# Performance work log

Hardware: AMD Instinct MI355X
Metric: run time of the kernel (lower is better)

Reference implementation:

```python
import jax, jax.numpy as jnp
import numpy as np

B, M, C = 8, 8192, 256   # batch, seeds, seed feature dim
F = 128                  # vote feature dim
P, K = 256, 32           # proposals, samples per group
CA, NCLS = 256, 10       # aggregated feat dim, classes
RADIUS = 0.3


def _lin(x, w, b):
    # 1x1 conv == pointwise linear; w: (out, in)
    return jnp.einsum('...c,oc->...o', x, w) + b


def _bnrelu(x, s, t):
    # eval-mode BatchNorm folded to per-channel affine, then ReLU
    return jnp.maximum(x * s + t, 0.0)


def _fps(xyz, npoint):
    # farthest point sampling; deterministic start at index 0
    Bb, N, _ = xyz.shape
    bidx = jnp.arange(Bb)

    def step(carry, _):
        distance, farthest = carry
        centroid = xyz[bidx, farthest][:, None, :]          # (B,1,2)
        d = jnp.sum((xyz - centroid) ** 2, -1)              # (B,N)
        distance = jnp.minimum(distance, d)
        return (distance, jnp.argmax(distance, -1)), farthest

    init = (jnp.full((Bb, N), 1e10, xyz.dtype), jnp.zeros((Bb,), jnp.int32))
    _, idx = jax.lax.scan(step, init, None, length=npoint)
    return jnp.transpose(idx)                               # (B, npoint)


def _ball_query(xyz, new_xyz, radius, nsample):
    # squared-distance cdist (monotone in euclid dist, so same sort order)
    N = xyz.shape[1]
    d2 = (jnp.sum(new_xyz ** 2, -1)[:, :, None]
          + jnp.sum(xyz ** 2, -1)[:, None, :]
          - 2.0 * jnp.einsum('bsd,bnd->bsn', new_xyz, xyz))  # (B,S,N)
    gidx = jnp.broadcast_to(jnp.arange(N), d2.shape)
    # out-of-radius points replaced by group_first (= index 0, as in source)
    gidx = jnp.where(d2 > radius * radius, 0, gidx)
    order = jnp.argsort(d2, axis=-1)
    return jnp.take_along_axis(gidx, order, axis=-1)[:, :, :nsample]


def _gather(points, idx):
    # points: (B,N,C); idx: (B,...) -> (B,...,C)
    return jax.vmap(lambda p, i: p[i])(points, idx)


def _forward(seed_xyz, seed_feats,
             v_off_w1, v_off_b1, v_off_s1, v_off_t1, v_off_w2, v_off_b2,
             v_ft_w1, v_ft_b1, v_ft_s1, v_ft_t1, v_ft_w2, v_ft_b2,
             a_w1, a_b1, a_s1, a_t1, a_w2, a_b2, a_s2, a_t2,
             p_w1, p_b1, p_s1, p_t1, p_w2, p_b2, p_s2, p_t2,
             obj_w, obj_b, cls_w, cls_b):
    # --- VotingModule (vote_factor=1) ---
    h = _bnrelu(_lin(seed_feats, v_off_w1, v_off_b1), v_off_s1, v_off_t1)
    offsets = _lin(h, v_off_w2, v_off_b2)                   # (B,M,2)
    g = _bnrelu(_lin(seed_feats, v_ft_w1, v_ft_b1), v_ft_s1, v_ft_t1)
    vote_feats = _lin(g, v_ft_w2, v_ft_b2)                  # (B,M,F)
    votes_xyz = seed_xyz + offsets                          # (B,M,2)

    # --- VoteAggregation ---
    fps_idx = _fps(votes_xyz, P)                            # (B,P)
    new_xyz = _gather(votes_xyz, fps_idx)                   # (B,P,2)
    gidx = _ball_query(votes_xyz, new_xyz, RADIUS, K)       # (B,P,K)
    gv = _gather(votes_xyz, gidx)                           # (B,P,K,2)
    gf = _gather(vote_feats, gidx)                          # (B,P,K,F)
    comb = jnp.concatenate([gv - new_xyz[:, :, None, :], gf], -1)  # (B,P,K,F+2)
    x = _bnrelu(_lin(comb, a_w1, a_b1), a_s1, a_t1)
    x = _bnrelu(_lin(x, a_w2, a_b2), a_s2, a_t2)
    pooled = jnp.max(x, axis=2)                             # (B,P,CA)

    # --- ProposalHead ---
    y = _bnrelu(_lin(pooled, p_w1, p_b1), p_s1, p_t1)
    y = _bnrelu(_lin(y, p_w2, p_b2), p_s2, p_t2)
    obj = _lin(y, obj_w, obj_b)[..., 0]                     # (B,P)
    cls = _lin(y, cls_w, cls_b)                             # (B,P,NCLS)
    return (new_xyz, obj, cls)


def setup_inputs() -> dict:
    key = jax.random.key(0)
    keys = iter(jax.random.split(key, 40))

    def w(shape):
        return (jax.random.normal(next(keys), shape) * 0.05).astype(jnp.float32)

    inp = {
        'seed_xyz': jax.random.uniform(next(keys), (B, M, 2), jnp.float32),
        'seed_feats': jax.random.normal(next(keys), (B, M, C), jnp.float32),
        # voting: offset branch
        'v_off_w1': w((C, C)), 'v_off_b1': w((C,)),
        'v_off_s1': 1.0 + w((C,)), 'v_off_t1': w((C,)),
        'v_off_w2': w((2, C)), 'v_off_b2': w((2,)),
        # voting: feature branch
        'v_ft_w1': w((C, C)), 'v_ft_b1': w((C,)),
        'v_ft_s1': 1.0 + w((C,)), 'v_ft_t1': w((C,)),
        'v_ft_w2': w((F, C)), 'v_ft_b2': w((F,)),
        # aggregation MLP
        'a_w1': w((CA, F + 2)), 'a_b1': w((CA,)),
        'a_s1': 1.0 + w((CA,)), 'a_t1': w((CA,)),
        'a_w2': w((CA, CA)), 'a_b2': w((CA,)),
        'a_s2': 1.0 + w((CA,)), 'a_t2': w((CA,)),
        # proposal head
        'p_w1': w((CA, CA)), 'p_b1': w((CA,)),
        'p_s1': 1.0 + w((CA,)), 'p_t1': w((CA,)),
        'p_w2': w((CA // 2, CA)), 'p_b2': w((CA // 2,)),
        'p_s2': 1.0 + w((CA // 2,)), 'p_t2': w((CA // 2,)),
        'obj_w': w((1, CA // 2)), 'obj_b': w((1,)),
        'cls_w': w((NCLS, CA // 2)), 'cls_b': w((NCLS,)),
    }
    return inp


def reference(seed_xyz, seed_feats,
              v_off_w1, v_off_b1, v_off_s1, v_off_t1, v_off_w2, v_off_b2,
              v_ft_w1, v_ft_b1, v_ft_s1, v_ft_t1, v_ft_w2, v_ft_b2,
              a_w1, a_b1, a_s1, a_t1, a_w2, a_b2, a_s2, a_t2,
              p_w1, p_b1, p_s1, p_t1, p_w2, p_b2, p_s2, p_t2,
              obj_w, obj_b, cls_w, cls_b):
    return _forward(seed_xyz, seed_feats,
                    v_off_w1, v_off_b1, v_off_s1, v_off_t1, v_off_w2, v_off_b2,
                    v_ft_w1, v_ft_b1, v_ft_s1, v_ft_t1, v_ft_w2, v_ft_b2,
                    a_w1, a_b1, a_s1, a_t1, a_w2, a_b2, a_s2, a_t2,
                    p_w1, p_b1, p_s1, p_t1, p_w2, p_b2, p_s2, p_t2,
                    obj_w, obj_b, cls_w, cls_b)
```

## Files before the change

kernel.cpp:

```cpp
#include <hip/hip_runtime.h>

typedef __attribute__((ext_vector_type(8))) short bf16x8;
typedef __attribute__((ext_vector_type(4))) float f32x4;
typedef unsigned short u16;
typedef unsigned int u32;
typedef unsigned long long u64;

#define DEV static __device__ __forceinline__
DEV u16 f2bf(float f) { u32 i = __float_as_uint(f); i += 0x7fffu + ((i >> 16) & 1u); return (u16)(i >> 16); }
DEV float bf2f(u16 u) { return __uint_as_float(((u32)u) << 16); }

constexpr int Mn = 8192;
constexpr int Pn = 256;
constexpr int Kn = 32;
constexpr float R2 = 0.09f;

__global__ __launch_bounds__(256) void k_voting_off(
    const float* __restrict__ sxyz,
    const float* __restrict__ sfeat,
    const float* __restrict__ ow1, const float* __restrict__ ob1,
    const float* __restrict__ os1, const float* __restrict__ ot1,
    const float* __restrict__ ow2, const float* __restrict__ ob2,
    float* __restrict__ votes)
{
  __shared__ float Xst[256][17];
  __shared__ float Hst[256][17];
  __shared__ float Wc[16][260];

  const int tid = threadIdx.x;
  const int row0 = blockIdx.x * 16;

  for (int i = tid; i < 16 * 256; i += 256) {
    int r = i >> 8, c = i & 255;
    Xst[c][r] = sfeat[(row0 + r) * 256 + c];
  }
  __syncthreads();

  const int rg = tid >> 6;
  const int ro = rg * 4;
  const int cg = tid & 63;

  float acc[4][4];
#pragma unroll
  for (int r = 0; r < 4; ++r)
#pragma unroll
    for (int j = 0; j < 4; ++j) acc[r][j] = 0.f;
  const int co = cg * 4;

  for (int kc = 0; kc < 16; ++kc) {
    __syncthreads();
    for (int i = tid; i < 256 * 16; i += 256) {
      int o = i >> 4, k = i & 15;
      Wc[k][o] = ow1[o * 256 + kc * 16 + k];
    }
    __syncthreads();
#pragma unroll
    for (int k = 0; k < 16; ++k) {
      const int kk = kc * 16 + k;
      float x[4], w[4];
#pragma unroll
      for (int r = 0; r < 4; ++r) x[r] = Xst[kk][ro + r];
#pragma unroll
      for (int j = 0; j < 4; ++j) w[j] = Wc[k][co + j];
#pragma unroll
      for (int r = 0; r < 4; ++r)
#pragma unroll
        for (int j = 0; j < 4; ++j)
          acc[r][j] = fmaf(x[r], w[j], acc[r][j]);
    }
  }
  __syncthreads();
#pragma unroll
  for (int j = 0; j < 4; ++j) {
    int o = co + j;
    float bb = ob1[o], ss = os1[o], tt = ot1[o];
#pragma unroll
    for (int r = 0; r < 4; ++r)
      Hst[o][ro + r] = fmaxf((acc[r][j] + bb) * ss + tt, 0.f);
  }
  __syncthreads();

  if (tid < 32) {
    int r = tid >> 1, o = tid & 1;
    float a = 0.f;
    for (int k = 0; k < 256; ++k)
      a = fmaf(Hst[k][r], ow2[o * 256 + k], a);
    a += ob2[o];
    int row = row0 + r;
    votes[row * 2 + o] = sxyz[row * 2 + o] + a;
  }
}

__global__ __launch_bounds__(512, 1) void k_fps(
    const float* __restrict__ votes, float* __restrict__ nxyz,
    float* __restrict__ out)
{
  const int b = blockIdx.x, tid = threadIdx.x;
  const float* vb = votes + b * Mn * 2;
  __shared__ float2 xy[Mn];
  __shared__ u32 Sd[2][32], Sl[2][32];
  __shared__ float histx[256], histy[256];

  {
    const float4* vb4 = (const float4*)vb;
#pragma unroll
    for (int j = tid; j < Mn / 2; j += 512) {
      float4 v = vb4[j];
      *(float4*)&xy[2 * j] = v;
    }
  }
  float dist[16];
#pragma unroll
  for (int s = 0; s < 16; ++s) dist[s] = 1e10f;
  __syncthreads();

  float cx = xy[0].x, cy = xy[0].y;
  if (tid == 0) { histx[0] = cx; histy[0] = cy; }

  for (int it = 1; it < Pn; ++it) {
    float bd = -1.f; int sb = 0;
#pragma unroll
    for (int s = 0; s < 16; ++s) {
      float2 p = xy[s * 512 + tid];
      float dx = p.x - cx, dy = p.y - cy;
      float d = fminf(dist[s], dx * dx + dy * dy);
      dist[s] = d;
      if (d > bd) { bd = d; sb = s; }
    }
    int bi = sb * 512 + tid;

    u32 hd = __float_as_uint(bd), hl = ~(u32)bi;

#define FPS_ROR(VD, VL, N)                                                      \
    {                                                                           \
      u32 od = (u32)__builtin_amdgcn_update_dpp(0, (int)VD, 0x120 + N, 0xF, 0xF, false); \
      u32 ol = (u32)__builtin_amdgcn_update_dpp(0, (int)VL, 0x120 + N, 0xF, 0xF, false); \
      bool g = (od > VD) || (od == VD && ol > VL);                              \
      VD = g ? od : VD; VL = g ? ol : VL;                                       \
    }
    FPS_ROR(hd, hl, 8)
    FPS_ROR(hd, hl, 4)
    FPS_ROR(hd, hl, 2)
    FPS_ROR(hd, hl, 1)

    const int buf = it & 1;
    if ((tid & 15) == 0) {
      int row = tid >> 4;
      Sd[buf][row] = hd; Sl[buf][row] = hl;
    }
    __syncthreads();

    int rr = tid & 15;
    u32 rd = Sd[buf][rr], rl = Sl[buf][rr];
    {
      u32 od = Sd[buf][16 + rr], ol = Sl[buf][16 + rr];
      bool g = (od > rd) || (od == rd && ol > rl);
      rd = g ? od : rd; rl = g ? ol : rl;
    }
    FPS_ROR(rd, rl, 8)
    FPS_ROR(rd, rl, 4)
    FPS_ROR(rd, rl, 2)
    FPS_ROR(rd, rl, 1)
#undef FPS_ROR

    int widx = (int)(~rl);
    float2 w = xy[widx];
    cx = w.x; cy = w.y;
    if (tid == 0) { histx[it] = cx; histy[it] = cy; }
  }
  __syncthreads();
  if (tid < 256) {
    float2 o2; o2.x = histx[tid]; o2.y = histy[tid];
    *(float2*)&nxyz[(b * Pn + tid) * 2] = o2;
    *(float2*)&out[(b * Pn + tid) * 2] = o2;
  }
}

__global__ __launch_bounds__(256) void k_ballq(
    const float* __restrict__ votes, const float* __restrict__ nxyz,
    int* __restrict__ gidx)
{
  const int bp = blockIdx.x, tid = threadIdx.x;
  const int b = bp >> 8;
  const float* vb = votes + b * Mn * 2;
  const float sx = nxyz[bp * 2], sy = nxyz[bp * 2 + 1];
  const float a = sx * sx + sy * sy;
  float d2[32];
#pragma unroll
  for (int s = 0; s < 32; ++s) {
    int i = tid * 32 + s;
    float x = vb[i * 2], y = vb[i * 2 + 1];
    d2[s] = (a + (x * x + y * y)) - 2.f * (sx * x + sy * y);
  }
  __shared__ float sd[4];
  __shared__ int si[4];
  __shared__ int swi;
  unsigned mask = 0;
  for (int kk = 0; kk < Kn; ++kk) {
    float bd = 3.4e38f; int bi = 0x7fffffff;
#pragma unroll
    for (int s = 0; s < 32; ++s)
      if (!((mask >> s) & 1u) && d2[s] < bd) { bd = d2[s]; bi = tid * 32 + s; }
#pragma unroll
    for (int off = 32; off > 0; off >>= 1) {
      float od = __shfl_xor(bd, off);
      int oi = __shfl_xor(bi, off);
      if (od < bd || (od == bd && oi < bi)) { bd = od; bi = oi; }
    }
    if ((tid & 63) == 0) { sd[tid >> 6] = bd; si[tid >> 6] = bi; }
    __syncthreads();
    if (tid == 0) {
#pragma unroll
      for (int w = 1; w < 4; ++w)
        if (sd[w] < bd || (sd[w] == bd && si[w] < bi)) { bd = sd[w]; bi = si[w]; }
      swi = bi;
      gidx[bp * Kn + kk] = (bd > R2) ? 0 : bi;
    }
    __syncthreads();
    int wi = swi;
    if ((wi >> 5) == tid) mask |= 1u << (wi & 31);
  }
}

__global__ __launch_bounds__(256) void k_prep(
    const float* __restrict__ fw1, const float* __restrict__ fw2,
    const float* __restrict__ aw1, const float* __restrict__ aw2,
    u16* __restrict__ FW1h, u16* __restrict__ FW2b,
    u16* __restrict__ AW1b, u16* __restrict__ AW2b)
{
  const int gid = blockIdx.x * 256 + threadIdx.x;
  const int gsz = gridDim.x * 256;
  for (int i = gid; i < 65536; i += gsz) FW1h[i] = f2bf(fw1[i]);
  for (int i = gid; i < 32768; i += gsz) FW2b[i] = f2bf(fw2[i]);
  for (int i = gid; i < 65536; i += gsz) AW2b[i] = f2bf(aw2[i]);
  for (int i = gid; i < 49152; i += gsz) {
    int o = i / 192, k = i % 192;
    AW1b[i] = (k < 130) ? f2bf(aw1[o * 130 + k]) : (u16)0;
  }
}

__global__ __launch_bounds__(256) void k_vf(
    const float* __restrict__ sfeat, const u16* __restrict__ FW1h,
    const float* __restrict__ fb1, const float* __restrict__ fs1,
    const float* __restrict__ ft1, const u16* __restrict__ FW2b,
    const float* __restrict__ fb2, u16* __restrict__ vfeat)
{
  __shared__ u16 Hs[128 * 136];
  __shared__ u16 As[128 * 40];
  __shared__ u16 Bs[128 * 40];
  const int tid = threadIdx.x;
  const int row0 = blockIdx.x * 128;
  const int wid = tid >> 6, lane = tid & 63, m16 = lane & 15, quad = lane >> 4;
  const int wr = wid >> 1, wc = wid & 1;
  const int sr = tid >> 1, sk = (tid & 1) * 16;

  f32x4 acc2[4][4];
#pragma unroll
  for (int mt = 0; mt < 4; ++mt)
#pragma unroll
    for (int nt = 0; nt < 4; ++nt) acc2[mt][nt] = (f32x4){0.f, 0.f, 0.f, 0.f};

  for (int h = 0; h < 2; ++h) {
    f32x4 acc[4][4];
#pragma unroll
    for (int mt = 0; mt < 4; ++mt)
#pragma unroll
      for (int nt = 0; nt < 4; ++nt) acc[mt][nt] = (f32x4){0.f, 0.f, 0.f, 0.f};

    for (int s = 0; s < 8; ++s) {
      __syncthreads();
      {
        const float* src = &sfeat[(row0 + sr) * 256 + s * 32 + sk];
        u32 packed[8];
#pragma unroll
        for (int q = 0; q < 4; ++q) {
          float4 v = *(const float4*)&src[q * 4];
          packed[q * 2]     = (u32)f2bf(v.x) | ((u32)f2bf(v.y) << 16);
          packed[q * 2 + 1] = (u32)f2bf(v.z) | ((u32)f2bf(v.w) << 16);
        }
        *(uint4*)&As[sr * 40 + sk]     = *(uint4*)&packed[0];
        *(uint4*)&As[sr * 40 + sk + 8] = *(uint4*)&packed[4];
        const u16* bsrc = &FW1h[(h * 128 + sr) * 256 + s * 32 + sk];
        *(uint4*)&Bs[sr * 40 + sk]     = *(const uint4*)&bsrc[0];
        *(uint4*)&Bs[sr * 40 + sk + 8] = *(const uint4*)&bsrc[8];
      }
      __syncthreads();
#pragma unroll
      for (int mt = 0; mt < 4; ++mt) {
        bf16x8 af = *(const bf16x8*)&As[(wr * 64 + mt * 16 + m16) * 40 + quad * 8];
#pragma unroll
        for (int nt = 0; nt < 4; ++nt) {
          bf16x8 bfr = *(const bf16x8*)&Bs[(wc * 64 + nt * 16 + m16) * 40 + quad * 8];
          acc[mt][nt] = __builtin_amdgcn_mfma_f32_16x16x32_bf16(af, bfr, acc[mt][nt], 0, 0, 0);
        }
      }
    }
    __syncthreads();
#pragma unroll
    for (int nt = 0; nt < 4; ++nt) {
      int colL = wc * 64 + nt * 16 + m16;
      int col = h * 128 + colL;
      float bb = fb1[col], ss = fs1[col], tt = ft1[col];
#pragma unroll
      for (int mt = 0; mt < 4; ++mt) {
        int rL = wr * 64 + mt * 16 + quad * 4;
#pragma unroll
        for (int r = 0; r < 4; ++r)
          Hs[(rL + r) * 136 + colL] = f2bf(fmaxf((acc[mt][nt][r] + bb) * ss + tt, 0.f));
      }
    }
    for (int s2 = 0; s2 < 4; ++s2) {
      __syncthreads();
      {
        const u16* bsrc = &FW2b[sr * 256 + h * 128 + s2 * 32 + sk];
        *(uint4*)&Bs[sr * 40 + sk]     = *(const uint4*)&bsrc[0];
        *(uint4*)&Bs[sr * 40 + sk + 8] = *(const uint4*)&bsrc[8];
      }
      __syncthreads();
#pragma unroll
      for (int mt = 0; mt < 4; ++mt) {
        bf16x8 af = *(const bf16x8*)&Hs[(wr * 64 + mt * 16 + m16) * 136 + s2 * 32 + quad * 8];
#pragma unroll
        for (int nt = 0; nt < 4; ++nt) {
          bf16x8 bfr = *(const bf16x8*)&Bs[(wc * 64 + nt * 16 + m16) * 40 + quad * 8];
          acc2[mt][nt] = __builtin_amdgcn_mfma_f32_16x16x32_bf16(af, bfr, acc2[mt][nt], 0, 0, 0);
        }
      }
    }
  }
#pragma unroll
  for (int nt = 0; nt < 4; ++nt) {
    int col = wc * 64 + nt * 16 + m16;
    float bb = fb2[col];
#pragma unroll
    for (int mt = 0; mt < 4; ++mt) {
      int rbase = row0 + wr * 64 + mt * 16 + quad * 4;
#pragma unroll
      for (int r = 0; r < 4; ++r)
        vfeat[(rbase + r) * 128 + col] = f2bf(acc2[mt][nt][r] + bb);
    }
  }
}

__global__ __launch_bounds__(256) void k_agg(
    const float* __restrict__ votes, const u16* __restrict__ vfeat,
    const float* __restrict__ nxyz, const int* __restrict__ gidx,
    const u16* __restrict__ AW1b, const float* __restrict__ ab1,
    const float* __restrict__ as1, const float* __restrict__ at1,
    const u16* __restrict__ AW2b, const float* __restrict__ ab2,
    const float* __restrict__ as2, const float* __restrict__ at2,
    float* __restrict__ pooled)
{
  __shared__ u16 U[32 * 264];
  __shared__ u16 Bs[256 * 72];
  __shared__ int gix[32];
  __shared__ float gvx[32], gvy[32];
  u16* CombA = U;
  u16* As = U;
  float* x2T = (float*)Bs;

  const int bp = blockIdx.x, tid = threadIdx.x, b = bp >> 8;
  if (tid < 32) {
    int g = gidx[bp * 32 + tid];
    gix[tid] = g;
    gvx[tid] = votes[(b * Mn + g) * 2];
    gvy[tid] = votes[(b * Mn + g) * 2 + 1];
  }
  __syncthreads();
  const float sx = nxyz[bp * 2], sy = nxyz[bp * 2 + 1];

  if (tid < 192) {
    int row = tid / 6, c = tid % 6;
    const u16* vsrc = &vfeat[(b * Mn + gix[row]) * 128];
    u16* dst = &CombA[row * 200 + c * 32];
    if (c == 0) {
      dst[0] = f2bf(gvx[row] - sx);
      dst[1] = f2bf(gvy[row] - sy);
      for (int k = 2; k < 32; ++k) dst[k] = vsrc[k - 2];
    } else if (c <= 3) {
      for (int k = 0; k < 32; ++k) dst[k] = vsrc[c * 32 + k - 2];
    } else if (c == 4) {
      dst[0] = vsrc[126]; dst[1] = vsrc[127];
      for (int k = 2; k < 32; ++k) dst[k] = 0;
    } else {
      for (int k = 0; k < 32; ++k) dst[k] = 0;
    }
  }

  const int wid = tid >> 6, lane = tid & 63, m16 = lane & 15, quad = lane >> 4;
  const int mt = wid & 1, nh = wid >> 1;

  f32x4 acc[8];
#pragma unroll
  for (int nt = 0; nt < 8; ++nt) acc[nt] = (f32x4){0.f, 0.f, 0.f, 0.f};
  for (int s = 0; s < 3; ++s) {
    __syncthreads();
    for (int i = tid; i < 4096; i += 256) {
      int n = i >> 4, c4 = i & 15;
      *(uint2*)&Bs[n * 72 + c4 * 4] = *(const uint2*)&AW1b[n * 192 + s * 64 + c4 * 4];
    }
    __syncthreads();
#pragma unroll
    for (int ks = 0; ks < 2; ++ks) {
      bf16x8 af = *(const bf16x8*)&CombA[(mt * 16 + m16) * 200 + s * 64 + ks * 32 + quad * 8];
#pragma unroll
      for (int nt = 0; nt < 8; ++nt) {
        bf16x8 bf_ = *(const bf16x8*)&Bs[(nh * 128 + nt * 16 + m16) * 72 + ks * 32 + quad * 8];
        acc[nt] = __builtin_amdgcn_mfma_f32_16x16x32_bf16(af, bf_, acc[nt], 0, 0, 0);
      }
    }
  }
  __syncthreads();
#pragma unroll
  for (int nt = 0; nt < 8; ++nt) {
    int col = nh * 128 + nt * 16 + m16;
    float bb = ab1[col], ss = as1[col], tt = at1[col];
#pragma unroll
    for (int r = 0; r < 4; ++r) {
      int samp = mt * 16 + quad * 4 + r;
      As[samp * 264 + col] = f2bf(fmaxf((acc[nt][r] + bb) * ss + tt, 0.f));
    }
  }

  f32x4 acc2[8];
#pragma unroll
  for (int nt = 0; nt < 8; ++nt) acc2[nt] = (f32x4){0.f, 0.f, 0.f, 0.f};
  for (int s = 0; s < 4; ++s) {
    __syncthreads();
    for (int i = tid; i < 4096; i += 256) {
      int n = i >> 4, c4 = i & 15;
      *(uint2*)&Bs[n * 72 + c4 * 4] = *(const uint2*)&AW2b[n * 256 + s * 64 + c4 * 4];
    }
    __syncthreads();
#pragma unroll
    for (int ks = 0; ks < 2; ++ks) {
      bf16x8 af = *(const bf16x8*)&As[(mt * 16 + m16) * 264 + s * 64 + ks * 32 + quad * 8];
#pragma unroll
      for (int nt = 0; nt < 8; ++nt) {
        bf16x8 bf_ = *(const bf16x8*)&Bs[(nh * 128 + nt * 16 + m16) * 72 + ks * 32 + quad * 8];
        acc2[nt] = __builtin_amdgcn_mfma_f32_16x16x32_bf16(af, bf_, acc2[nt], 0, 0, 0);
      }
    }
  }
  __syncthreads();
#pragma unroll
  for (int nt = 0; nt < 8; ++nt) {
    int col = nh * 128 + nt * 16 + m16;
    float bb = ab2[col], ss = as2[col], tt = at2[col];
#pragma unroll
    for (int r = 0; r < 4; ++r) {
      int samp = mt * 16 + quad * 4 + r;
      x2T[col * 33 + samp] = fmaxf((acc2[nt][r] + bb) * ss + tt, 0.f);
    }
  }
  __syncthreads();
  {
    float m = x2T[tid * 33];
#pragma unroll
    for (int s2 = 1; s2 < 32; ++s2) m = fmaxf(m, x2T[tid * 33 + s2]);
    pooled[bp * 256 + tid] = m;
  }
}

__global__ __launch_bounds__(256) void k_head(
    const float* __restrict__ pooled,
    const float* __restrict__ pw1, const float* __restrict__ pb1,
    const float* __restrict__ ps1, const float* __restrict__ pt1,
    const float* __restrict__ pw2, const float* __restrict__ pb2,
    const float* __restrict__ ps2, const float* __restrict__ pt2,
    const float* __restrict__ objw, const float* __restrict__ objb,
    const float* __restrict__ clsw, const float* __restrict__ clsb,
    float* __restrict__ out)
{
  __shared__ float xr[256], y1[256], y2[128];
  const int bp = blockIdx.x, tid = threadIdx.x;
  xr[tid] = pooled[bp * 256 + tid];
  __syncthreads();
  {
    float a = 0.f;
    for (int c = 0; c < 256; ++c) a = fmaf(xr[c], pw1[tid * 256 + c], a);
    a = (a + pb1[tid]) * ps1[tid] + pt1[tid];
    y1[tid] = fmaxf(a, 0.f);
  }
  __syncthreads();
  if (tid < 128) {
    float a = 0.f;
    for (int c = 0; c < 256; ++c) a = fmaf(y1[c], pw2[tid * 256 + c], a);
    a = (a + pb2[tid]) * ps2[tid] + pt2[tid];
    y2[tid] = fmaxf(a, 0.f);
  }
  __syncthreads();
  if (tid < 10) {
    float a = 0.f;
    for (int c = 0; c < 128; ++c) a = fmaf(y2[c], clsw[tid * 128 + c], a);
    out[6144 + bp * 10 + tid] = a + clsb[tid];
  } else if (tid == 10) {
    float a = 0.f;
    for (int c = 0; c < 128; ++c) a = fmaf(y2[c], objw[c], a);
    out[4096 + bp] = a + objb[0];
  }
}

extern "C" void kernel_launch(void* const* d_in, const int* in_sizes, int n_in,
                              void* d_out, int out_size, void* d_ws, size_t ws_size,
                              hipStream_t stream)
{
  (void)in_sizes; (void)n_in; (void)out_size; (void)ws_size;
  const float* sxyz  = (const float*)d_in[0];
  const float* sfeat = (const float*)d_in[1];
  const float* ow1 = (const float*)d_in[2];
  const float* ob1 = (const float*)d_in[3];
  const float* os1 = (const float*)d_in[4];
  const float* ot1 = (const float*)d_in[5];
  const float* ow2 = (const float*)d_in[6];
  const float* ob2 = (const float*)d_in[7];
  const float* fw1 = (const float*)d_in[8];
  const float* fb1 = (const float*)d_in[9];
  const float* fs1 = (const float*)d_in[10];
  const float* ft1 = (const float*)d_in[11];
  const float* fw2 = (const float*)d_in[12];
  const float* fb2 = (const float*)d_in[13];
  const float* aw1 = (const float*)d_in[14];
  const float* ab1 = (const float*)d_in[15];
  const float* as1 = (const float*)d_in[16];
  const float* at1 = (const float*)d_in[17];
  const float* aw2 = (const float*)d_in[18];
  const float* ab2 = (const float*)d_in[19];
  const float* as2 = (const float*)d_in[20];
  const float* at2 = (const float*)d_in[21];
  const float* pw1 = (const float*)d_in[22];
  const float* pb1 = (const float*)d_in[23];
  const float* ps1 = (const float*)d_in[24];
  const float* pt1 = (const float*)d_in[25];
  const float* pw2 = (const float*)d_in[26];
  const float* pb2 = (const float*)d_in[27];
  const float* ps2 = (const float*)d_in[28];
  const float* pt2 = (const float*)d_in[29];
  const float* objw = (const float*)d_in[30];
  const float* objb = (const float*)d_in[31];
  const float* clsw = (const float*)d_in[32];
  const float* clsb = (const float*)d_in[33];

  char* ws = (char*)d_ws;
  float* votes  = (float*)(ws + 0);
  u16*   vfeat  = (u16*)  (ws + 524288);
  float* nxyz   = (float*)(ws + 17301504);
  int*   gidxp  = (int*)  (ws + 17317888);
  float* pooled = (float*)(ws + 17580032);
  u16*   FW1h   = (u16*)  (ws + 19677184);
  u16*   FW2b   = (u16*)  (ws + 19808256);
  u16*   AW1b   = (u16*)  (ws + 19873792);
  u16*   AW2b   = (u16*)  (ws + 19972096);
  float* out    = (float*)d_out;

  k_voting_off<<<dim3(4096), dim3(256), 0, stream>>>(
      sxyz, sfeat, ow1, ob1, os1, ot1, ow2, ob2, votes);

  k_fps<<<dim3(8), dim3(512), 0, stream>>>(votes, nxyz, out);

  k_ballq<<<dim3(2048), dim3(256), 0, stream>>>(votes, nxyz, gidxp);

  k_prep<<<dim3(256), dim3(256), 0, stream>>>(
      fw1, fw2, aw1, aw2, FW1h, FW2b, AW1b, AW2b);

  k_vf<<<dim3(512), dim3(256), 0, stream>>>(
      sfeat, FW1h, fb1, fs1, ft1, FW2b, fb2, vfeat);

  k_agg<<<dim3(2048), dim3(256), 0, stream>>>(
      votes, vfeat, nxyz, gidxp, AW1b, ab1, as1, at1,
      AW2b, ab2, as2, at2, pooled);

  k_head<<<dim3(2048), dim3(256), 0, stream>>>(
      pooled, pw1, pb1, ps1, pt1, pw2, pb2, ps2, pt2,
      objw, objb, clsw, clsb, out);
}
```

Before: 947.5 us.

## Prefetch FPS points into registers, split the argmax, and vectorize voting LDS reads

In the FPS loop, each thread's 16 point coordinates now sit in registers. The next iteration's LDS reads are issued after the distance update, so their latency can overlap the cross-lane and cross-wave argmax reduction. The per-thread argmax becomes four independent chunk maxima combined at the end, which shortens the serial compare chain while keeping the first-index tie rule. The voting-offset GEMM reads X and W from padded LDS arrays with float2 loads and a strided column mapping, to cut LDS instruction count and bank conflicts. The cost is higher register pressure in the FPS kernel and an LDS reload every iteration.

After: 971.3 us. 1.03x slower.

```diff
diff --git a/kernel.cpp b/kernel.cpp
--- a/kernel.cpp
+++ b/kernel.cpp
@@ -23,9 +23,9 @@
     const float* __restrict__ ow2, const float* __restrict__ ob2,
     float* __restrict__ votes)
 {
-  __shared__ float Xst[256][17];
-  __shared__ float Hst[256][17];
-  __shared__ float Wc[16][260];
+  __shared__ __align__(16) float Xst[256][18];
+  __shared__ __align__(16) float Hst[256][17];
+  __shared__ __align__(16) float Wc[16][262];
 
   const int tid = threadIdx.x;
   const int row0 = blockIdx.x * 16;
@@ -45,7 +45,6 @@
   for (int r = 0; r < 4; ++r)
 #pragma unroll
     for (int j = 0; j < 4; ++j) acc[r][j] = 0.f;
-  const int co = cg * 4;
 
   for (int kc = 0; kc < 16; ++kc) {
     __syncthreads();
@@ -57,11 +56,12 @@
 #pragma unroll
     for (int k = 0; k < 16; ++k) {
       const int kk = kc * 16 + k;
-      float x[4], w[4];
-#pragma unroll
-      for (int r = 0; r < 4; ++r) x[r] = Xst[kk][ro + r];
-#pragma unroll
-      for (int j = 0; j < 4; ++j) w[j] = Wc[k][co + j];
+      float2 xlo = *(const float2*)&Xst[kk][ro];
+      float2 xhi = *(const float2*)&Xst[kk][ro + 2];
+      float2 wlo = *(const float2*)&Wc[k][2 * cg];
+      float2 whi = *(const float2*)&Wc[k][128 + 2 * cg];
+      float x[4] = {xlo.x, xlo.y, xhi.x, xhi.y};
+      float w[4] = {wlo.x, wlo.y, whi.x, whi.y};
 #pragma unroll
       for (int r = 0; r < 4; ++r)
 #pragma unroll
@@ -72,7 +72,7 @@
   __syncthreads();
 #pragma unroll
   for (int j = 0; j < 4; ++j) {
-    int o = co + j;
+    int o = (j < 2) ? (2 * cg + j) : (126 + 2 * cg + j);
     float bb = ob1[o], ss = os1[o], tt = ot1[o];
 #pragma unroll
     for (int r = 0; r < 4; ++r)
@@ -97,7 +97,7 @@
 {
   const int b = blockIdx.x, tid = threadIdx.x;
   const float* vb = votes + b * Mn * 2;
-  __shared__ float2 xy[Mn];
+  __shared__ __align__(16) float2 xy[Mn];
   __shared__ u32 Sd[2][32], Sl[2][32];
   __shared__ float histx[256], histy[256];
 
@@ -105,8 +105,7 @@
     const float4* vb4 = (const float4*)vb;
 #pragma unroll
     for (int j = tid; j < Mn / 2; j += 512) {
-      float4 v = vb4[j];
-      *(float4*)&xy[2 * j] = v;
+      *(float4*)&xy[2 * j] = vb4[j];
     }
   }
   float dist[16];
@@ -117,18 +116,44 @@
   float cx = xy[0].x, cy = xy[0].y;
   if (tid == 0) { histx[0] = cx; histy[0] = cy; }
 
+  float pxr[16], pyr[16];
+#pragma unroll
+  for (int s = 0; s < 16; ++s) {
+    float2 p = xy[s * 512 + tid];
+    pxr[s] = p.x; pyr[s] = p.y;
+  }
+#pragma unroll
+  for (int s = 0; s < 16; ++s) asm volatile("" : "+v"(pxr[s]), "+v"(pyr[s]));
+
   for (int it = 1; it < Pn; ++it) {
-    float bd = -1.f; int sb = 0;
+    float bdc[4]; int sbc[4];
+#pragma unroll
+    for (int c = 0; c < 4; ++c) {
+      float bdl = -1.f; int sbl = 4 * c;
+#pragma unroll
+      for (int q = 0; q < 4; ++q) {
+        int s = 4 * c + q;
+        float dx = pxr[s] - cx, dy = pyr[s] - cy;
+        float d = fminf(dist[s], dx * dx + dy * dy);
+        dist[s] = d;
+        if (d > bdl) { bdl = d; sbl = s; }
+      }
+      bdc[c] = bdl; sbc[c] = sbl;
+    }
+    float bd = bdc[0]; int sb = sbc[0];
+    if (bdc[1] > bd) { bd = bdc[1]; sb = sbc[1]; }
+    if (bdc[2] > bd) { bd = bdc[2]; sb = sbc[2]; }
+    if (bdc[3] > bd) { bd = bdc[3]; sb = sbc[3]; }
+
 #pragma unroll
     for (int s = 0; s < 16; ++s) {
       float2 p = xy[s * 512 + tid];
-      float dx = p.x - cx, dy = p.y - cy;
-      float d = fminf(dist[s], dx * dx + dy * dy);
-      dist[s] = d;
-      if (d > bd) { bd = d; sb = s; }
-    }
+      pxr[s] = p.x; pyr[s] = p.y;
+    }
+#pragma unroll
+    for (int s = 0; s < 16; ++s) asm volatile("" : "+v"(pxr[s]), "+v"(pyr[s]));
+
     int bi = sb * 512 + tid;
-
     u32 hd = __float_as_uint(bd), hl = ~(u32)bi;
 
 #define FPS_ROR(VD, VL, N)                                                      \
```

## Enlarge voting-offset GEMM tile to 32 rows and stream input chunks

Applied to the files above, without the earlier changes.

The vote offset kernel now handles 32 seed rows per block instead of 16, with each thread computing an 8x4 accumulator tile. Input features are staged per 16-wide k-chunk alongside the weight chunk rather than preloaded in full, and shared-memory reads use float2 vector loads. The larger tile halves how often the 256x256 weight matrix is reloaded into shared memory, since half as many blocks are launched. In exchange the kernel uses more registers per thread and keeps fewer blocks in flight.

Measured after the change: 938.2 us. About the same (-1.0%).

```diff
diff --git a/kernel.cpp b/kernel.cpp
--- a/kernel.cpp
+++ b/kernel.cpp
@@ -15,7 +15,7 @@
 constexpr int Kn = 32;
 constexpr float R2 = 0.09f;
 
-__global__ __launch_bounds__(256) void k_voting_off(
+__global__ __launch_bounds__(256, 2) void k_voting_off(
     const float* __restrict__ sxyz,
     const float* __restrict__ sfeat,
     const float* __restrict__ ow1, const float* __restrict__ ob1,
@@ -23,29 +23,22 @@
     const float* __restrict__ ow2, const float* __restrict__ ob2,
     float* __restrict__ votes)
 {
-  __shared__ float Xst[256][17];
-  __shared__ float Hst[256][17];
-  __shared__ float Wc[16][260];
+  __shared__ __align__(16) float Xc[16][34];
+  __shared__ __align__(16) float Wc[16][262];
+  __shared__ __align__(16) float Hst[256][33];
 
   const int tid = threadIdx.x;
-  const int row0 = blockIdx.x * 16;
-
-  for (int i = tid; i < 16 * 256; i += 256) {
-    int r = i >> 8, c = i & 255;
-    Xst[c][r] = sfeat[(row0 + r) * 256 + c];
-  }
-  __syncthreads();
-
-  const int rg = tid >> 6;
-  const int ro = rg * 4;
+  const int row0 = blockIdx.x * 32;
+
+  const int wv = tid >> 6;
+  const int w8 = wv * 8;
   const int cg = tid & 63;
 
-  float acc[4][4];
-#pragma unroll
-  for (int r = 0; r < 4; ++r)
+  float acc[8][4];
+#pragma unroll
+  for (int r = 0; r < 8; ++r)
 #pragma unroll
     for (int j = 0; j < 4; ++j) acc[r][j] = 0.f;
-  const int co = cg * 4;
 
   for (int kc = 0; kc < 16; ++kc) {
     __syncthreads();
@@ -53,17 +46,23 @@
       int o = i >> 4, k = i & 15;
       Wc[k][o] = ow1[o * 256 + kc * 16 + k];
     }
+    for (int i = tid; i < 32 * 16; i += 256) {
+      int r = i >> 4, k = i & 15;
+      Xc[k][r] = sfeat[(row0 + r) * 256 + kc * 16 + k];
+    }
     __syncthreads();
 #pragma unroll
     for (int k = 0; k < 16; ++k) {
-      const int kk = kc * 16 + k;
-      float x[4], w[4];
-#pragma unroll
-      for (int r = 0; r < 4; ++r) x[r] = Xst[kk][ro + r];
-#pragma unroll
-      for (int j = 0; j < 4; ++j) w[j] = Wc[k][co + j];
-#pragma unroll
-      for (int r = 0; r < 4; ++r)
+      float2 x01 = *(const float2*)&Xc[k][w8];
+      float2 x23 = *(const float2*)&Xc[k][w8 + 2];
+      float2 x45 = *(const float2*)&Xc[k][w8 + 4];
+      float2 x67 = *(const float2*)&Xc[k][w8 + 6];
+      float2 wlo = *(const float2*)&Wc[k][2 * cg];
+      float2 whi = *(const float2*)&Wc[k][128 + 2 * cg];
+      float x[8] = {x01.x, x01.y, x23.x, x23.y, x45.x, x45.y, x67.x, x67.y};
+      float w[4] = {wlo.x, wlo.y, whi.x, whi.y};
+#pragma unroll
+      for (int r = 0; r < 8; ++r)
 #pragma unroll
         for (int j = 0; j < 4; ++j)
           acc[r][j] = fmaf(x[r], w[j], acc[r][j]);
@@ -72,15 +71,15 @@
   __syncthreads();
 #pragma unroll
   for (int j = 0; j < 4; ++j) {
-    int o = co + j;
+    int o = (j < 2) ? (2 * cg + j) : (126 + 2 * cg + j);
     float bb = ob1[o], ss = os1[o], tt = ot1[o];
 #pragma unroll
-    for (int r = 0; r < 4; ++r)
-      Hst[o][ro + r] = fmaxf((acc[r][j] + bb) * ss + tt, 0.f);
-  }
-  __syncthreads();
-
-  if (tid < 32) {
+    for (int r = 0; r < 8; ++r)
+      Hst[o][w8 + r] = fmaxf((acc[r][j] + bb) * ss + tt, 0.f);
+  }
+  __syncthreads();
+
+  if (tid < 64) {
     int r = tid >> 1, o = tid & 1;
     float a = 0.f;
     for (int k = 0; k < 256; ++k)
@@ -553,7 +552,7 @@
   u16*   AW2b   = (u16*)  (ws + 19972096);
   float* out    = (float*)d_out;
 
-  k_voting_off<<<dim3(4096), dim3(256), 0, stream>>>(
+  k_voting_off<<<dim3(2048), dim3(256), 0, stream>>>(
       sxyz, sfeat, ow1, ob1, os1, ot1, ow2, ob2, votes);
 
   k_fps<<<dim3(8), dim3(512), 0, stream>>>(votes, nxyz, out);
```
